# Kernel tuning notes

Measured on AMD Instinct MI355X. Metric: run time of the kernel, lower is better.

## Reference

```python
import jax, jax.numpy as jnp
import numpy as np

INPUT_SIZE = 1024
HIDDEN = 2048
B = 4096


def setup_inputs() -> dict:
    key = jax.random.key(0)
    ks = jax.random.split(key, 11)
    D = INPUT_SIZE + HIDDEN
    bound = 1.0 / np.sqrt(D)  # nn.Linear default init range
    def lin(kw, kb):
        W = jax.random.uniform(kw, (HIDDEN, D), jnp.float32, -bound, bound)
        b = jax.random.uniform(kb, (HIDDEN,), jnp.float32, -bound, bound)
        return W, b
    W_i, b_i = lin(ks[0], ks[1])
    W_f, b_f = lin(ks[2], ks[3])
    W_c, b_c = lin(ks[4], ks[5])
    W_o, b_o = lin(ks[6], ks[7])
    x_t = jax.random.normal(ks[8], (B, INPUT_SIZE), jnp.float32)
    h_prev = jax.random.normal(ks[9], (B, HIDDEN), jnp.float32)
    c_prev = jax.random.normal(ks[10], (B, HIDDEN), jnp.float32)
    return {
        "x_t": x_t, "h_prev": h_prev, "c_prev": c_prev,
        "W_i": W_i, "b_i": b_i, "W_f": W_f, "b_f": b_f,
        "W_c": W_c, "b_c": b_c, "W_o": W_o, "b_o": b_o,
    }


def reference(x_t, h_prev, c_prev, W_i, b_i, W_f, b_f, W_c, b_c, W_o, b_o):
    # combined: [B, input+hidden]
    combined = jnp.concatenate([x_t, h_prev], axis=1)
    # fused gate GEMM: stack the four weight matrices -> one [D, 4H] matmul
    W_all = jnp.concatenate([W_i, W_f, W_c, W_o], axis=0)  # [4H, D]
    b_all = jnp.concatenate([b_i, b_f, b_c, b_o], axis=0)  # [4H]
    gates = combined @ W_all.T + b_all                     # [B, 4H]
    gi, gf, gc, go = jnp.split(gates, 4, axis=1)
    i_t = jax.nn.sigmoid(gi)
    f_t = jax.nn.sigmoid(gf)
    g_t = jnp.tanh(gc)
    o_t = jax.nn.sigmoid(go)
    c_t = f_t * c_prev + i_t * g_t
    h_t = o_t * jnp.tanh(c_t)
    # dropout is identity in eval / p=0
    return (h_t, c_t)
```

## Files before the change

kernel.cpp:

```cpp
#include <hip/hip_runtime.h>
#include <stdint.h>

#define B_DIM 4096
#define IN_SZ 1024
#define HID   2048
#define D_DIM 3072
#define BM 256
#define BN 64
#define BK 64
#define NT (D_DIM / BK)

typedef float  f32x4  __attribute__((ext_vector_type(4)));
typedef short  short8 __attribute__((ext_vector_type(8)));

__device__ __forceinline__ unsigned short f2bf(float f) {
    union { float f; unsigned u; } v; v.f = f;
    unsigned u = v.u + 0x7fffu + ((v.u >> 16) & 1u);
    return (unsigned short)(u >> 16);
}

__device__ __forceinline__ void async_load16(const void* g, void* l) {
    __builtin_amdgcn_global_load_lds(
        (const __attribute__((address_space(1))) unsigned int*)g,
        (__attribute__((address_space(3))) unsigned int*)l,
        16, 0, 0);
}

__device__ __forceinline__ float sigm(float x) {
    return 1.0f / (1.0f + __expf(-x));
}
__device__ __forceinline__ float tanh_f(float x) {
    return 1.0f - 2.0f / (__expf(2.0f * x) + 1.0f);
}

__global__ __launch_bounds__(256)
void convert_all(const float* __restrict__ x, const float* __restrict__ h,
                 const float* __restrict__ W0, const float* __restrict__ W1,
                 const float* __restrict__ W2, const float* __restrict__ W3,
                 unsigned short* __restrict__ Abf, unsigned short* __restrict__ Wbf) {
    const int NA = B_DIM * D_DIM / 8;
    const int NW = 4 * HID * D_DIM / 8;
    int idx = blockIdx.x * blockDim.x + threadIdx.x;
    const float* src;
    unsigned short* dst;
    if (idx < NA) {
        const int C8 = D_DIM / 8;
        int b = idx / C8, c8 = idx - b * C8;
        src = (c8 < IN_SZ / 8) ? x + (size_t)b * IN_SZ + c8 * 8
                               : h + (size_t)b * HID + (c8 - IN_SZ / 8) * 8;
        dst = Abf + (size_t)idx * 8;
    } else {
        int wi = idx - NA;
        if (wi >= NW) return;
        const int PG = HID * D_DIM / 8;
        int g = wi / PG, r = wi - g * PG;
        const float* W = (g == 0) ? W0 : (g == 1) ? W1 : (g == 2) ? W2 : W3;
        src = W + (size_t)r * 8;
        dst = Wbf + (size_t)wi * 8;
    }
    float4 v0 = ((const float4*)src)[0];
    float4 v1 = ((const float4*)src)[1];
    short8 o;
    o[0] = (short)f2bf(v0.x); o[1] = (short)f2bf(v0.y);
    o[2] = (short)f2bf(v0.z); o[3] = (short)f2bf(v0.w);
    o[4] = (short)f2bf(v1.x); o[5] = (short)f2bf(v1.y);
    o[6] = (short)f2bf(v1.z); o[7] = (short)f2bf(v1.w);
    *(short8*)dst = o;
}

template <int IB>
__device__ __forceinline__ void read_a(short8 (&aR)[4][2], const char* smA,
                                       int aBase, int sw0, int sw1) {
#pragma unroll
    for (int i = 0; i < 4; ++i) {
        aR[i][0] = *(const short8*)(smA + aBase + (IB + i) * 2048 + sw0);
        aR[i][1] = *(const short8*)(smA + aBase + (IB + i) * 2048 + sw1);
    }
}

template <int JB>
__device__ __forceinline__ void read_b(short8 (&bR)[4][2], const char* smB,
                                       int bBase, int sw0, int sw1) {
#pragma unroll
    for (int j = 0; j < 2; ++j) {
        bR[JB + j][0] = *(const short8*)(smB + bBase + (JB + j) * 2048 + sw0);
        bR[JB + j][1] = *(const short8*)(smB + bBase + (JB + j) * 2048 + sw1);
    }
}

template <int IB, int JB>
__device__ __forceinline__ void mfma_quad(f32x4 (&acc)[8][4], const short8 (&aR)[4][2],
                                          const short8 (&bR)[4][2]) {
#pragma unroll
    for (int i = 0; i < 4; ++i)
#pragma unroll
        for (int j = 0; j < 2; ++j)
#pragma unroll
            for (int s = 0; s < 2; ++s)
                acc[IB + i][JB + j] = __builtin_amdgcn_mfma_f32_16x16x32_bf16(
                    aR[i][s], bR[JB + j][s], acc[IB + i][JB + j], 0, 0, 0);
}

__global__ __launch_bounds__(512, 2)
void lstm_gemm(const unsigned short* __restrict__ Abf,
               const unsigned short* __restrict__ Wbf,
               const float* __restrict__ b_i, const float* __restrict__ b_f,
               const float* __restrict__ b_c, const float* __restrict__ b_o,
               const float* __restrict__ c_prev,
               float* __restrict__ h_out, float* __restrict__ c_out) {
    extern __shared__ char sm[];

    const int tid  = threadIdx.x;
    const int lane = tid & 63;
    const int wave = tid >> 6;
    const int wm   = wave >> 2;
    const int wn   = wave & 3;
    const int l16  = lane & 15;
    const int quad = lane >> 4;
    const int r7   = l16 & 7;

    const int m0 = blockIdx.x * BM;
    const int h0 = blockIdx.y * BN;

    const int g8 = lane >> 3;
    const int sl = (lane & 7) ^ g8;
    const unsigned short* srcA[4];
    const unsigned short* srcB[4];
#pragma unroll
    for (int i = 0; i < 4; ++i) {
        const int rt = (wave * 4 + i) * 8 + g8;
        srcA[i] = Abf + (size_t)(m0 + rt) * D_DIM + sl * 8;
        const int grow = ((rt >> 4) & 3) * HID + h0 + (rt >> 6) * 16 + (rt & 15);
        srcB[i] = Wbf + (size_t)grow * D_DIM + sl * 8;
    }
    const int chunk = wave * 4096;

    const int aBase = (wm * 128 + l16) * 128;
    const int bBase = (wn * 64  + l16) * 128;
    const int sw0 = ((0 * 4 + quad) ^ r7) * 16;
    const int sw1 = ((1 * 4 + quad) ^ r7) * 16;

    f32x4 acc[8][4] = {};
    short8 aR[4][2], bR[4][2];

#pragma unroll
    for (int i = 0; i < 4; ++i) {
        async_load16(srcA[i], sm + chunk + i * 1024);
        async_load16(srcB[i], sm + 32768 + chunk + i * 1024);
    }
    asm volatile("s_waitcnt vmcnt(0)" ::: "memory");
    __builtin_amdgcn_s_barrier();

    for (int kt = 0; kt < NT; ++kt) {
        const char* smA = sm + (kt & 1) * 65536;
        const char* smB = smA + 32768;
        char* smAn = sm + ((kt + 1) & 1) * 65536;
        char* smBn = smAn + 32768;
        const int koff = (kt + 1) * BK;
        const bool pf = (kt + 1 < NT);

        if (pf) {
#pragma unroll
            for (int i = 0; i < 4; ++i)
                async_load16(srcA[i] + koff, smAn + chunk + i * 1024);
        }
        read_a<0>(aR, smA, aBase, sw0, sw1);
        read_b<0>(bR, smB, bBase, sw0, sw1);
        __builtin_amdgcn_s_barrier();
        asm volatile("s_waitcnt lgkmcnt(0)" ::: "memory");
        __builtin_amdgcn_sched_barrier(0);
        __builtin_amdgcn_s_setprio(1);
        mfma_quad<0, 0>(acc, aR, bR);
        __builtin_amdgcn_s_setprio(0);
        __builtin_amdgcn_s_barrier();

        if (pf) {
#pragma unroll
            for (int i = 0; i < 4; ++i)
                async_load16(srcB[i] + koff, smBn + chunk + i * 1024);
        }
        read_b<2>(bR, smB, bBase, sw0, sw1);
        __builtin_amdgcn_s_barrier();
        asm volatile("s_waitcnt lgkmcnt(0)" ::: "memory");
        __builtin_amdgcn_sched_barrier(0);
        __builtin_amdgcn_s_setprio(1);
        mfma_quad<0, 2>(acc, aR, bR);
        __builtin_amdgcn_s_setprio(0);
        __builtin_amdgcn_s_barrier();

        read_a<4>(aR, smA, aBase, sw0, sw1);
        __builtin_amdgcn_s_barrier();
        asm volatile("s_waitcnt lgkmcnt(0)" ::: "memory");
        __builtin_amdgcn_sched_barrier(0);
        __builtin_amdgcn_s_setprio(1);
        mfma_quad<4, 2>(acc, aR, bR);
        __builtin_amdgcn_s_setprio(0);
        __builtin_amdgcn_s_barrier();

        __builtin_amdgcn_sched_barrier(0);
        __builtin_amdgcn_s_setprio(1);
        mfma_quad<4, 0>(acc, aR, bR);
        __builtin_amdgcn_s_setprio(0);
        asm volatile("s_waitcnt vmcnt(0)" ::: "memory");
        __builtin_amdgcn_s_barrier();
    }

    const int h = h0 + wn * 16 + l16;
    const float biv = b_i[h], bfv = b_f[h], bcv = b_c[h], bov = b_o[h];
    const int mb = m0 + wm * 128 + quad * 4;
#pragma unroll
    for (int i = 0; i < 8; ++i) {
#pragma unroll
        for (int r = 0; r < 4; ++r) {
            const int m = mb + i * 16 + r;
            const size_t off = (size_t)m * HID + h;
            const float gi = acc[i][0][r] + biv;
            const float gf = acc[i][1][r] + bfv;
            const float gc = acc[i][2][r] + bcv;
            const float go = acc[i][3][r] + bov;
            const float it = sigm(gi), ft = sigm(gf);
            const float gt = tanh_f(gc), ot = sigm(go);
            const float c = ft * c_prev[off] + it * gt;
            h_out[off] = ot * tanh_f(c);
            c_out[off] = c;
        }
    }
}

extern "C" void kernel_launch(void* const* d_in, const int* in_sizes, int n_in,
                              void* d_out, int out_size, void* d_ws, size_t ws_size,
                              hipStream_t stream) {
    const float* x_t    = (const float*)d_in[0];
    const float* h_prev = (const float*)d_in[1];
    const float* c_prev = (const float*)d_in[2];
    const float* W_i = (const float*)d_in[3];
    const float* b_i = (const float*)d_in[4];
    const float* W_f = (const float*)d_in[5];
    const float* b_f = (const float*)d_in[6];
    const float* W_c = (const float*)d_in[7];
    const float* b_c = (const float*)d_in[8];
    const float* W_o = (const float*)d_in[9];
    const float* b_o = (const float*)d_in[10];
    float* out = (float*)d_out;

    unsigned short* Abf = (unsigned short*)d_ws;
    unsigned short* Wbf = (unsigned short*)((char*)d_ws + (size_t)B_DIM * D_DIM * 2);

    static bool s_attr = false;
    if (!s_attr) {
        (void)hipFuncSetAttribute((const void*)lstm_gemm,
                                  hipFuncAttributeMaxDynamicSharedMemorySize, 131072);
        s_attr = true;
    }

    {
        const int n = (B_DIM * D_DIM + 4 * HID * D_DIM) / 8;
        convert_all<<<n / 256, 256, 0, stream>>>(x_t, h_prev, W_i, W_f, W_c, W_o,
                                                 Abf, Wbf);
    }
    dim3 grid(B_DIM / BM, HID / BN);
    lstm_gemm<<<grid, 512, 131072, stream>>>(Abf, Wbf, b_i, b_f, b_c, b_o, c_prev,
                                             out, out + (size_t)B_DIM * HID);
}
```

Before: 387.3 us.

## Deepen global-to-LDS prefetch to two tiles ahead with partial vmcnt waits

Restructures the K loop so global loads for tile kt+2 are issued into the buffer currently being consumed, after its reads finish, and the loop waits only for the older batch (vmcnt(8)) instead of draining all loads each iteration. The prologue preloads two tiles and the last two iterations are peeled with no prefetch. This is meant to hide more global memory latency behind the MFMA work. The cost is in-place buffer reuse that depends on barrier ordering to avoid overwriting data still being read.

```diff
diff --git a/kernel.cpp b/kernel.cpp
--- a/kernel.cpp
+++ b/kernel.cpp
@@ -101,6 +101,65 @@
                     aR[i][s], bR[JB + j][s], acc[IB + i][JB + j], 0, 0, 0);
 }
 
+template <int MODE>
+__device__ __forceinline__ void tile_body(
+    f32x4 (&acc)[8][4], short8 (&aR)[4][2], short8 (&bR)[4][2],
+    const char* smA, const char* smB,
+    const unsigned short* const* srcA, const unsigned short* const* srcB,
+    int koff, int chunk, int aBase, int bBase, int sw0, int sw1) {
+    char* stA = (char*)smA + chunk;
+    char* stB = (char*)smB + chunk;
+
+    read_a<0>(aR, smA, aBase, sw0, sw1);
+    read_b<0>(bR, smB, bBase, sw0, sw1);
+    __builtin_amdgcn_s_barrier();
+    asm volatile("s_waitcnt lgkmcnt(0)" ::: "memory");
+    __builtin_amdgcn_sched_barrier(0);
+    __builtin_amdgcn_s_setprio(1);
+    mfma_quad<0, 0>(acc, aR, bR);
+    __builtin_amdgcn_s_setprio(0);
+    __builtin_amdgcn_s_barrier();
+
+    read_b<2>(bR, smB, bBase, sw0, sw1);
+    __builtin_amdgcn_s_barrier();
+    asm volatile("s_waitcnt lgkmcnt(0)" ::: "memory");
+    __builtin_amdgcn_sched_barrier(0);
+    __builtin_amdgcn_s_setprio(1);
+    mfma_quad<0, 2>(acc, aR, bR);
+    __builtin_amdgcn_s_setprio(0);
+    __builtin_amdgcn_s_barrier();
+
+    if (MODE == 1) {
+#pragma unroll
+        for (int i = 0; i < 4; ++i)
+            async_load16(srcB[i] + koff, stB + i * 1024);
+    }
+    read_a<4>(aR, smA, aBase, sw0, sw1);
+    __builtin_amdgcn_s_barrier();
+    asm volatile("s_waitcnt lgkmcnt(0)" ::: "memory");
+    __builtin_amdgcn_sched_barrier(0);
+    __builtin_amdgcn_s_setprio(1);
+    mfma_quad<4, 2>(acc, aR, bR);
+    __builtin_amdgcn_s_setprio(0);
+    __builtin_amdgcn_s_barrier();
+
+    if (MODE == 1) {
+#pragma unroll
+        for (int i = 0; i < 4; ++i)
+            async_load16(srcA[i] + koff, stA + i * 1024);
+    }
+    __builtin_amdgcn_sched_barrier(0);
+    __builtin_amdgcn_s_setprio(1);
+    mfma_quad<4, 0>(acc, aR, bR);
+    __builtin_amdgcn_s_setprio(0);
+    if (MODE == 1) {
+        asm volatile("s_waitcnt vmcnt(8)" ::: "memory");
+    } else if (MODE == 0) {
+        asm volatile("s_waitcnt vmcnt(0)" ::: "memory");
+    }
+    if (MODE >= 0) __builtin_amdgcn_s_barrier();
+}
+
 __global__ __launch_bounds__(512, 2)
 void lstm_gemm(const unsigned short* __restrict__ Abf,
                const unsigned short* __restrict__ Wbf,
@@ -145,64 +204,31 @@
 
 #pragma unroll
     for (int i = 0; i < 4; ++i) {
-        async_load16(srcA[i], sm + chunk + i * 1024);
-        async_load16(srcB[i], sm + 32768 + chunk + i * 1024);
-    }
-    asm volatile("s_waitcnt vmcnt(0)" ::: "memory");
-    __builtin_amdgcn_s_barrier();
-
-    for (int kt = 0; kt < NT; ++kt) {
+        async_load16(srcB[i],      sm + 32768 + chunk + i * 1024);
+        async_load16(srcA[i],      sm + chunk + i * 1024);
+    }
+#pragma unroll
+    for (int i = 0; i < 4; ++i) {
+        async_load16(srcB[i] + BK, sm + 65536 + 32768 + chunk + i * 1024);
+        async_load16(srcA[i] + BK, sm + 65536 + chunk + i * 1024);
+    }
+    asm volatile("s_waitcnt vmcnt(8)" ::: "memory");
+    __builtin_amdgcn_s_barrier();
+
+    for (int kt = 0; kt < NT - 2; ++kt) {
         const char* smA = sm + (kt & 1) * 65536;
-        const char* smB = smA + 32768;
-        char* smAn = sm + ((kt + 1) & 1) * 65536;
-        char* smBn = smAn + 32768;
-        const int koff = (kt + 1) * BK;
-        const bool pf = (kt + 1 < NT);
-
-        if (pf) {
-#pragma unroll
-            for (int i = 0; i < 4; ++i)
-                async_load16(srcA[i] + koff, smAn + chunk + i * 1024);
-        }
-        read_a<0>(aR, smA, aBase, sw0, sw1);
-        read_b<0>(bR, smB, bBase, sw0, sw1);
-        __builtin_amdgcn_s_barrier();
-        asm volatile("s_waitcnt lgkmcnt(0)" ::: "memory");
-        __builtin_amdgcn_sched_barrier(0);
-        __builtin_amdgcn_s_setprio(1);
-        mfma_quad<0, 0>(acc, aR, bR);
-        __builtin_amdgcn_s_setprio(0);
-        __builtin_amdgcn_s_barrier();
-
-        if (pf) {
-#pragma unroll
-            for (int i = 0; i < 4; ++i)
-                async_load16(srcB[i] + koff, smBn + chunk + i * 1024);
-        }
-        read_b<2>(bR, smB, bBase, sw0, sw1);
-        __builtin_amdgcn_s_barrier();
-        asm volatile("s_waitcnt lgkmcnt(0)" ::: "memory");
-        __builtin_amdgcn_sched_barrier(0);
-        __builtin_amdgcn_s_setprio(1);
-        mfma_quad<0, 2>(acc, aR, bR);
-        __builtin_amdgcn_s_setprio(0);
-        __builtin_amdgcn_s_barrier();
-
-        read_a<4>(aR, smA, aBase, sw0, sw1);
-        __builtin_amdgcn_s_barrier();
-        asm volatile("s_waitcnt lgkmcnt(0)" ::: "memory");
-        __builtin_amdgcn_sched_barrier(0);
-        __builtin_amdgcn_s_setprio(1);
-        mfma_quad<4, 2>(acc, aR, bR);
-        __builtin_amdgcn_s_setprio(0);
-        __builtin_amdgcn_s_barrier();
-
-        __builtin_amdgcn_sched_barrier(0);
-        __builtin_amdgcn_s_setprio(1);
-        mfma_quad<4, 0>(acc, aR, bR);
-        __builtin_amdgcn_s_setprio(0);
-        asm volatile("s_waitcnt vmcnt(0)" ::: "memory");
-        __builtin_amdgcn_s_barrier();
+        tile_body<1>(acc, aR, bR, smA, smA + 32768, srcA, srcB,
+                     (kt + 2) * BK, chunk, aBase, bBase, sw0, sw1);
+    }
+    {
+        const char* smA = sm + ((NT - 2) & 1) * 65536;
+        tile_body<0>(acc, aR, bR, smA, smA + 32768, srcA, srcB,
+                     0, chunk, aBase, bBase, sw0, sw1);
+    }
+    {
+        const char* smA = sm + ((NT - 1) & 1) * 65536;
+        tile_body<-1>(acc, aR, bR, smA, smA + 32768, srcA, srcB,
+                      0, chunk, aBase, bBase, sw0, sw1);
     }
 
     const int h = h0 + wn * 16 + l16;
```

New measurement: 385.3 us. No clear change (-0.5%).

## Restructure GEMM main loop into register-pipelined K-half stages with fewer barriers

Applied to the files above, without the earlier changes.

Reorganizes the bf16 MFMA inner loop so each K tile is processed in four 4x4 MFMA blocks split by K-half, with LDS fragment reads for the next block issued while the current block computes. The first fragments of the next tile are prefetched before the last MFMA block, and the per-phase barriers and lgkmcnt waits are removed, leaving two barriers per tile. The last tile is peeled out of the loop. The aim is to hide LDS read latency and cut synchronization stalls, at the cost of more live registers and reliance on compiler-inserted waits for correctness.

```diff
diff --git a/kernel.cpp b/kernel.cpp
--- a/kernel.cpp
+++ b/kernel.cpp
@@ -69,36 +69,86 @@
 }
 
 template <int IB>
-__device__ __forceinline__ void read_a(short8 (&aR)[4][2], const char* smA,
-                                       int aBase, int sw0, int sw1) {
-#pragma unroll
-    for (int i = 0; i < 4; ++i) {
-        aR[i][0] = *(const short8*)(smA + aBase + (IB + i) * 2048 + sw0);
-        aR[i][1] = *(const short8*)(smA + aBase + (IB + i) * 2048 + sw1);
-    }
-}
-
-template <int JB>
-__device__ __forceinline__ void read_b(short8 (&bR)[4][2], const char* smB,
-                                       int bBase, int sw0, int sw1) {
-#pragma unroll
-    for (int j = 0; j < 2; ++j) {
-        bR[JB + j][0] = *(const short8*)(smB + bBase + (JB + j) * 2048 + sw0);
-        bR[JB + j][1] = *(const short8*)(smB + bBase + (JB + j) * 2048 + sw1);
-    }
-}
-
-template <int IB, int JB>
-__device__ __forceinline__ void mfma_quad(f32x4 (&acc)[8][4], const short8 (&aR)[4][2],
-                                          const short8 (&bR)[4][2]) {
-#pragma unroll
-    for (int i = 0; i < 4; ++i)
-#pragma unroll
-        for (int j = 0; j < 2; ++j)
-#pragma unroll
-            for (int s = 0; s < 2; ++s)
-                acc[IB + i][JB + j] = __builtin_amdgcn_mfma_f32_16x16x32_bf16(
-                    aR[i][s], bR[JB + j][s], acc[IB + i][JB + j], 0, 0, 0);
+__device__ __forceinline__ void mfma16(f32x4 (&acc)[8][4], const short8 (&a)[4],
+                                       const short8 (&b)[4]) {
+#pragma unroll
+    for (int i = 0; i < 4; ++i)
+#pragma unroll
+        for (int j = 0; j < 4; ++j)
+            acc[IB + i][j] = __builtin_amdgcn_mfma_f32_16x16x32_bf16(
+                a[i], b[j], acc[IB + i][j], 0, 0, 0);
+}
+
+template <int MODE>
+__device__ __forceinline__ void tile_body(
+    f32x4 (&acc)[8][4],
+    short8 (&a0s0)[4], short8 (&a1s0)[4], short8 (&a0s1)[4], short8 (&a1s1)[4],
+    short8 (&bs0)[4], short8 (&bs1)[4],
+    const char* cur, char* nxt,
+    const unsigned short* srcA0, const unsigned short* const* srcB,
+    int koff, int chunk, int aBase, int bBase, int sw0, int sw1) {
+    const char* curA = cur;
+    const char* curB = cur + 32768;
+
+    if (MODE) {
+#pragma unroll
+        for (int i = 0; i < 4; ++i)
+            async_load16(srcA0 + i * 8 * D_DIM + koff, nxt + chunk + i * 1024);
+    }
+#pragma unroll
+    for (int i = 0; i < 4; ++i)
+        a1s0[i] = *(const short8*)(curA + aBase + (4 + i) * 2048 + sw0);
+    bs1[0] = *(const short8*)(curB + bBase + 0 * 2048 + sw1);
+    bs1[1] = *(const short8*)(curB + bBase + 1 * 2048 + sw1);
+    __builtin_amdgcn_sched_barrier(0);
+    __builtin_amdgcn_s_setprio(1);
+    mfma16<0>(acc, a0s0, bs0);
+    __builtin_amdgcn_s_setprio(0);
+
+    if (MODE) {
+#pragma unroll
+        for (int i = 0; i < 4; ++i)
+            async_load16(srcB[i] + koff, nxt + 32768 + chunk + i * 1024);
+    }
+    bs1[2] = *(const short8*)(curB + bBase + 2 * 2048 + sw1);
+    bs1[3] = *(const short8*)(curB + bBase + 3 * 2048 + sw1);
+#pragma unroll
+    for (int i = 0; i < 4; ++i)
+        a0s1[i] = *(const short8*)(curA + aBase + i * 2048 + sw1);
+    __builtin_amdgcn_sched_barrier(0);
+    __builtin_amdgcn_s_setprio(1);
+    mfma16<4>(acc, a1s0, bs0);
+    __builtin_amdgcn_s_setprio(0);
+
+#pragma unroll
+    for (int i = 0; i < 4; ++i)
+        a1s1[i] = *(const short8*)(curA + aBase + (4 + i) * 2048 + sw1);
+    __builtin_amdgcn_sched_barrier(0);
+    __builtin_amdgcn_s_setprio(1);
+    mfma16<0>(acc, a0s1, bs1);
+    __builtin_amdgcn_s_setprio(0);
+    if (MODE) {
+        asm volatile("s_waitcnt vmcnt(0)" ::: "memory");
+        __builtin_amdgcn_s_barrier();
+        asm volatile("" ::: "memory");
+    }
+
+    if (MODE) {
+#pragma unroll
+        for (int i = 0; i < 4; ++i)
+            a0s0[i] = *(const short8*)(nxt + aBase + i * 2048 + sw0);
+#pragma unroll
+        for (int j = 0; j < 4; ++j)
+            bs0[j] = *(const short8*)(nxt + 32768 + bBase + j * 2048 + sw0);
+    }
+    __builtin_amdgcn_sched_barrier(0);
+    __builtin_amdgcn_s_setprio(1);
+    mfma16<4>(acc, a1s1, bs1);
+    __builtin_amdgcn_s_setprio(0);
+    if (MODE) {
+        __builtin_amdgcn_s_barrier();
+        asm volatile("" ::: "memory");
+    }
 }
 
 __global__ __launch_bounds__(512, 2)
@@ -124,12 +174,11 @@
 
     const int g8 = lane >> 3;
     const int sl = (lane & 7) ^ g8;
-    const unsigned short* srcA[4];
+    const unsigned short* srcA0 = Abf + (size_t)(m0 + wave * 32 + g8) * D_DIM + sl * 8;
     const unsigned short* srcB[4];
 #pragma unroll
     for (int i = 0; i < 4; ++i) {
-        const int rt = (wave * 4 + i) * 8 + g8;
-        srcA[i] = Abf + (size_t)(m0 + rt) * D_DIM + sl * 8;
+        const int rt = wave * 32 + i * 8 + g8;
         const int grow = ((rt >> 4) & 3) * HID + h0 + (rt >> 6) * 16 + (rt & 15);
         srcB[i] = Wbf + (size_t)grow * D_DIM + sl * 8;
     }
@@ -141,69 +190,32 @@
     const int sw1 = ((1 * 4 + quad) ^ r7) * 16;
 
     f32x4 acc[8][4] = {};
-    short8 aR[4][2], bR[4][2];
+    short8 a0s0[4], a1s0[4], a0s1[4], a1s1[4], bs0[4], bs1[4];
 
 #pragma unroll
     for (int i = 0; i < 4; ++i) {
-        async_load16(srcA[i], sm + chunk + i * 1024);
         async_load16(srcB[i], sm + 32768 + chunk + i * 1024);
+        async_load16(srcA0 + i * 8 * D_DIM, sm + chunk + i * 1024);
     }
     asm volatile("s_waitcnt vmcnt(0)" ::: "memory");
     __builtin_amdgcn_s_barrier();
-
-    for (int kt = 0; kt < NT; ++kt) {
-        const char* smA = sm + (kt & 1) * 65536;
-        const char* smB = smA + 32768;
-        char* smAn = sm + ((kt + 1) & 1) * 65536;
-        char* smBn = smAn + 32768;
-        const int koff = (kt + 1) * BK;
-        const bool pf = (kt + 1 < NT);
-
-        if (pf) {
-#pragma unroll
-            for (int i = 0; i < 4; ++i)
-                async_load16(srcA[i] + koff, smAn + chunk + i * 1024);
-        }
-        read_a<0>(aR, smA, aBase, sw0, sw1);
-        read_b<0>(bR, smB, bBase, sw0, sw1);
-        __builtin_amdgcn_s_barrier();
-        asm volatile("s_waitcnt lgkmcnt(0)" ::: "memory");
-        __builtin_amdgcn_sched_barrier(0);
-        __builtin_amdgcn_s_setprio(1);
-        mfma_quad<0, 0>(acc, aR, bR);
-        __builtin_amdgcn_s_setprio(0);
-        __builtin_amdgcn_s_barrier();
-
-        if (pf) {
-#pragma unroll
-            for (int i = 0; i < 4; ++i)
-                async_load16(srcB[i] + koff, smBn + chunk + i * 1024);
-        }
-        read_b<2>(bR, smB, bBase, sw0, sw1);
-        __builtin_amdgcn_s_barrier();
-        asm volatile("s_waitcnt lgkmcnt(0)" ::: "memory");
-        __builtin_amdgcn_sched_barrier(0);
-        __builtin_amdgcn_s_setprio(1);
-        mfma_quad<0, 2>(acc, aR, bR);
-        __builtin_amdgcn_s_setprio(0);
-        __builtin_amdgcn_s_barrier();
-
-        read_a<4>(aR, smA, aBase, sw0, sw1);
-        __builtin_amdgcn_s_barrier();
-        asm volatile("s_waitcnt lgkmcnt(0)" ::: "memory");
-        __builtin_amdgcn_sched_barrier(0);
-        __builtin_amdgcn_s_setprio(1);
-        mfma_quad<4, 2>(acc, aR, bR);
-        __builtin_amdgcn_s_setprio(0);
-        __builtin_amdgcn_s_barrier();
-
-        __builtin_amdgcn_sched_barrier(0);
-        __builtin_amdgcn_s_setprio(1);
-        mfma_quad<4, 0>(acc, aR, bR);
-        __builtin_amdgcn_s_setprio(0);
-        asm volatile("s_waitcnt vmcnt(0)" ::: "memory");
-        __builtin_amdgcn_s_barrier();
-    }
+    asm volatile("" ::: "memory");
+#pragma unroll
+    for (int i = 0; i < 4; ++i)
+        a0s0[i] = *(const short8*)(sm + aBase + i * 2048 + sw0);
+#pragma unroll
+    for (int j = 0; j < 4; ++j)
+        bs0[j] = *(const short8*)(sm + 32768 + bBase + j * 2048 + sw0);
+
+    for (int kt = 0; kt < NT - 1; ++kt) {
+        const char* cur = sm + (kt & 1) * 65536;
+        char* nxt = (char*)sm + ((kt + 1) & 1) * 65536;
+        tile_body<1>(acc, a0s0, a1s0, a0s1, a1s1, bs0, bs1, cur, nxt,
+                     srcA0, srcB, (kt + 1) * BK, chunk, aBase, bBase, sw0, sw1);
+    }
+    tile_body<0>(acc, a0s0, a1s0, a0s1, a1s1, bs0, bs1,
+                 sm + ((NT - 1) & 1) * 65536, (char*)sm,
+                 srcA0, srcB, 0, chunk, aBase, bBase, sw0, sw1);
 
     const int h = h0 + wn * 16 + l16;
     const float biv = b_i[h], bfv = b_f[h], bcv = b_c[h], bov = b_o[h];
```

Measured after the change: 378.7 us. 2.2% less time.
